# Kernel tuning notes

Hardware: AMD Instinct MI355X
Metric: run time of the kernel (lower is better)

## Reference

```python
import jax, jax.numpy as jnp
import numpy as np

N, E, F_IN, C = 50000, 800000, 128, 300
NEG_SLOPE = 0.2  # PyG GATv2Conv default negative_slope


def setup_inputs() -> dict:
    key = jax.random.key(0)
    ks = jax.random.split(key, 10)
    x = jax.random.normal(ks[0], (N, F_IN), dtype=jnp.float32)
    edge_index = jax.random.randint(ks[1], (2, E), 0, N, dtype=jnp.int64)
    s_in = np.float32(1.0 / np.sqrt(F_IN))
    s_c = np.float32(1.0 / np.sqrt(C))
    Wl = jax.random.normal(ks[2], (F_IN, C), dtype=jnp.float32) * s_in
    bl = jnp.zeros((C,), jnp.float32)
    Wr = jax.random.normal(ks[3], (F_IN, C), dtype=jnp.float32) * s_in
    br = jnp.zeros((C,), jnp.float32)
    att = jax.random.normal(ks[4], (C,), dtype=jnp.float32) * s_c
    bias = jnp.zeros((C,), jnp.float32)
    lw = jax.random.normal(ks[5], (C, 1), dtype=jnp.float32) * s_c
    lb = jnp.zeros((1,), jnp.float32)
    return {"x": x, "edge_index": edge_index, "Wl": Wl, "bl": bl,
            "Wr": Wr, "br": br, "att": att, "bias": bias, "lw": lw, "lb": lb}


def reference(x, edge_index, Wl, bl, Wr, br, att, bias, lw, lb):
    n = x.shape[0]
    # GATv2: separate source/target linear transforms
    xl = x @ Wl + bl  # [N, C] (source / message features)
    xr = x @ Wr + br  # [N, C] (target features)
    # add self loops (PyG default add_self_loops=True)
    loops = jnp.arange(n, dtype=edge_index.dtype)
    src = jnp.concatenate([edge_index[0], loops])  # [E+N]
    dst = jnp.concatenate([edge_index[1], loops])  # [E+N]
    # GATv2 attention logit: a^T LeakyReLU(xl_j + xr_i)
    e = jax.nn.leaky_relu(xl[src] + xr[dst], NEG_SLOPE) @ att  # [E+N]
    # segment softmax over incoming edges of each target node
    m = jax.ops.segment_max(e, dst, num_segments=n)
    ex = jnp.exp(e - m[dst])
    denom = jax.ops.segment_sum(ex, dst, num_segments=n)
    alpha = ex / denom[dst]  # [E+N]
    # weighted scatter-aggregation of source messages + conv bias
    out = jax.ops.segment_sum(xl[src] * alpha[:, None], dst, num_segments=n) + bias
    h = jax.nn.relu(out)          # torch.relu
    # F.dropout in eval mode is identity (reference is inference math)
    return jax.nn.sigmoid(h @ lw + lb)  # [N, 1]
```

## Files before the change

kernel.cpp:

```cpp
#include <hip/hip_runtime.h>
#include <hip/hip_fp16.h>

#define F_IN 128
#define C_DIM 300
#define NEG_SLOPE 0.2f
#define NCT  38
#define CH   8
#define NPB  256

typedef _Float16 half8 __attribute__((ext_vector_type(8)));
typedef _Float16 half4 __attribute__((ext_vector_type(4)));
typedef _Float16 h2    __attribute__((ext_vector_type(2)));
typedef float    f32x4 __attribute__((ext_vector_type(4)));
typedef float    f32x2 __attribute__((ext_vector_type(2)));

__device__ inline h2 as_h2(unsigned u) { union { unsigned u; h2 h; } c; c.u = u; return c.h; }
__device__ inline unsigned as_u(h2 h)  { union { unsigned u; h2 h; } c; c.h = h; return c.u; }
__device__ inline f32x2 upv(unsigned u) {
    h2 h = as_h2(u);
    f32x2 r; r.x = (float)h.x; r.y = (float)h.y; return r;
}

#if __has_builtin(__builtin_amdgcn_fdot2)
__device__ inline float fdot2w(h2 a, h2 b, float c) {
    return __builtin_amdgcn_fdot2(a, b, c, false);
}
#else
__device__ inline float fdot2w(h2 a, h2 b, float c) {
    return fmaf((float)a.y, (float)b.y, fmaf((float)a.x, (float)b.x, c));
}
#endif

__global__ __launch_bounds__(256) void convert_w(
    const float* __restrict__ Wl, const float* __restrict__ Wr,
    _Float16* __restrict__ Bp)
{
    int idx = blockIdx.x * 256 + threadIdx.x;
    if (idx >= 608 * F_IN) return;
    int nn = idx % 608;
    int k  = idx / 608;
    float v = 0.f;
    if (nn < 300)                   v = Wl[k * C_DIM + nn];
    else if (nn >= 304 && nn < 604) v = Wr[k * C_DIM + (nn - 304)];
    int ct = nn >> 4, n16 = nn & 15;
    int kr = k & 31,  ks  = k >> 5;
    int lane = ((kr >> 3) << 4) | n16;
    int j = k & 7;
    Bp[((((ct * 4 + ks) * 64) + lane) << 3) | j] = (_Float16)v;
}

__global__ __launch_bounds__(256) void gemm_xlxr(
    const float* __restrict__ x, const _Float16* __restrict__ Bp,
    const float* __restrict__ bl, const float* __restrict__ br,
    _Float16* __restrict__ xlh, _Float16* __restrict__ xrh, int n)
{
    __shared__ __align__(16) _Float16 xs[64][136];
    const int rb0 = blockIdx.x * 64;
    const int t   = threadIdx.x;

    #pragma unroll
    for (int i = 0; i < 8; ++i) {
        int flat = (i * 256 + t) * 4;
        int r = flat >> 7;
        int k = flat & 127;
        int gr = rb0 + r;
        if (gr >= n) gr = n - 1;
        float4 v = *reinterpret_cast<const float4*>(x + (size_t)gr * F_IN + k);
        half4 h = { (_Float16)v.x, (_Float16)v.y, (_Float16)v.z, (_Float16)v.w };
        *reinterpret_cast<half4*>(&xs[r][k]) = h;
    }
    __syncthreads();

    const int w    = t >> 6;
    const int lane = t & 63;
    const int m    = lane & 15;
    const int quad = lane >> 4;

    half8 a[4];
    #pragma unroll
    for (int ks = 0; ks < 4; ++ks)
        a[ks] = *reinterpret_cast<const half8*>(&xs[w * 16 + m][ks * 32 + quad * 8]);

    const int rbase = rb0 + w * 16 + quad * 4;

    #pragma unroll 2
    for (int ct = 0; ct < NCT; ++ct) {
        f32x4 acc = {0.f, 0.f, 0.f, 0.f};
        #pragma unroll
        for (int ks = 0; ks < 4; ++ks) {
            half8 b = *reinterpret_cast<const half8*>(
                Bp + (((size_t)(ct * 4 + ks) * 64 + lane) << 3));
            acc = __builtin_amdgcn_mfma_f32_16x16x32_f16(a[ks], b, acc, 0, 0, 0);
        }
        int col = ct * 16 + m;
        int isL = (col < 300);
        int isR = (col >= 304 && col < 604);
        if (isL | isR) {
            float bv = isL ? bl[col] : br[col - 304];
            _Float16* tab = isL ? (xlh + col) : (xrh + (col - 304));
            #pragma unroll
            for (int reg = 0; reg < 4; ++reg) {
                int row = rbase + reg;
                if (row < n)
                    tab[(size_t)row * C_DIM] = (_Float16)(acc[reg] + bv);
            }
        }
    }
}

__global__ __launch_bounds__(256) void bucket_count(
    const int* __restrict__ dst, unsigned* __restrict__ bcnt, int nE, int chunk4)
{
    __shared__ unsigned cnt[256];
    const int b = blockIdx.x, t = threadIdx.x;
    cnt[t] = 0;
    __syncthreads();
    const int4* dst4 = reinterpret_cast<const int4*>(dst);
    const int total4 = (nE + 3) >> 2;
    const int lo = b * chunk4;
    const int hi = min(total4, lo + chunk4);
    for (int i = lo + t; i < hi; i += 256) {
        int4 d = dst4[i];
        int e = i * 4;
        if (e + 3 < nE) {
            atomicAdd(&cnt[d.x >> 8], 1u);
            atomicAdd(&cnt[d.y >> 8], 1u);
            atomicAdd(&cnt[d.z >> 8], 1u);
            atomicAdd(&cnt[d.w >> 8], 1u);
        } else {
            if (e < nE)     atomicAdd(&cnt[d.x >> 8], 1u);
            if (e + 1 < nE) atomicAdd(&cnt[d.y >> 8], 1u);
            if (e + 2 < nE) atomicAdd(&cnt[d.z >> 8], 1u);
        }
    }
    __syncthreads();
    bcnt[t * NPB + b] = cnt[t];
}

__global__ __launch_bounds__(256) void scan_part(
    const unsigned* __restrict__ counts, unsigned* __restrict__ bsum, int n)
{
    __shared__ unsigned s[256];
    const int t = threadIdx.x;
    const int base = blockIdx.x * 1024 + t * 4;
    unsigned v = 0;
    #pragma unroll
    for (int i = 0; i < 4; ++i) {
        int idx = base + i;
        if (idx < n) v += counts[idx];
    }
    s[t] = v;
    __syncthreads();
    for (int off = 128; off > 0; off >>= 1) {
        if (t < off) s[t] += s[t + off];
        __syncthreads();
    }
    if (t == 0) bsum[blockIdx.x] = s[0];
}

__global__ __launch_bounds__(256) void scan_final(
    const unsigned* __restrict__ counts, const unsigned* __restrict__ bsum,
    unsigned* __restrict__ offs, int n, int nblk)
{
    __shared__ unsigned s[256];
    __shared__ unsigned sbase;
    const int t = threadIdx.x;
    if (t < 64) {
        unsigned v64 = (t < nblk) ? bsum[t] : 0u;
        unsigned inc = v64;
        #pragma unroll
        for (int off = 1; off < 64; off <<= 1) {
            unsigned u = __shfl_up(inc, off);
            if (t >= off) inc += u;
        }
        if (t == (int)blockIdx.x) sbase = inc - v64;
        if (blockIdx.x == gridDim.x - 1 && t == 63) offs[n] = inc;
    }
    const int base = blockIdx.x * 1024 + t * 4;
    unsigned c[4];
    unsigned v = 0;
    #pragma unroll
    for (int i = 0; i < 4; ++i) {
        int idx = base + i;
        c[i] = (idx < n) ? counts[idx] : 0u;
        v += c[i];
    }
    s[t] = v;
    __syncthreads();
    for (int off = 1; off < 256; off <<= 1) {
        unsigned u = (t >= off) ? s[t - off] : 0u;
        __syncthreads();
        if (t >= off) s[t] += u;
        __syncthreads();
    }
    unsigned run = sbase + s[t] - v;
    #pragma unroll
    for (int i = 0; i < 4; ++i) {
        int idx = base + i;
        if (idx < n) {
            offs[idx] = run;
            run += c[i];
        }
    }
}

__global__ __launch_bounds__(256) void partition_edges(
    const int* __restrict__ src, const int* __restrict__ dst,
    const unsigned* __restrict__ boff,
    unsigned* __restrict__ ebuf, int nE, int chunk4)
{
    __shared__ unsigned cur[256];
    const int b = blockIdx.x, t = threadIdx.x;
    cur[t] = boff[t * NPB + b];
    __syncthreads();
    const int4* dst4 = reinterpret_cast<const int4*>(dst);
    const int4* src4 = reinterpret_cast<const int4*>(src);
    const int total4 = (nE + 3) >> 2;
    const int lo = b * chunk4;
    const int hi = min(total4, lo + chunk4);
    for (int i = lo + t; i < hi; i += 256) {
        int4 d = dst4[i];
        int4 s = src4[i];
        int e = i * 4;
        int dv[4] = {d.x, d.y, d.z, d.w};
        int sv[4] = {s.x, s.y, s.z, s.w};
        #pragma unroll
        for (int j = 0; j < 4; ++j) {
            if (e + j < nE) {
                unsigned p = atomicAdd(&cur[dv[j] >> 8], 1u);
                ebuf[p] = (unsigned)sv[j] | ((unsigned)(dv[j] & 255) << 16);
            }
        }
    }
}

__global__ __launch_bounds__(256) void bucket_csr(
    const unsigned* __restrict__ ebuf, const unsigned* __restrict__ boff,
    unsigned* __restrict__ offs, int* __restrict__ csr_src, int n, int nE, int nb)
{
    __shared__ unsigned cnt[256];
    __shared__ unsigned s[256];
    __shared__ unsigned cur[256];
    const int bk = blockIdx.x;
    const int t  = threadIdx.x;
    const unsigned bstart = boff[(unsigned)bk * NPB];
    const unsigned bend   = boff[(unsigned)(bk + 1) * NPB];
    cnt[t] = 0;
    __syncthreads();
    for (unsigned i = bstart + t; i < bend; i += 256)
        atomicAdd(&cnt[(ebuf[i] >> 16) & 255], 1u);
    __syncthreads();
    unsigned v = cnt[t];
    s[t] = v;
    __syncthreads();
    for (int off = 1; off < 256; off <<= 1) {
        unsigned u = (t >= off) ? s[t - off] : 0u;
        __syncthreads();
        if (t >= off) s[t] += u;
        __syncthreads();
    }
    const unsigned excl = s[t] - v;
    const int node = (bk << 8) + t;
    if (node <= n) offs[node] = bstart + excl;
    if (t == 0 && bk == nb - 1 && (n & 255) == 0) offs[n] = (unsigned)nE;
    cur[t] = bstart + excl;
    __syncthreads();
    for (unsigned i = bstart + t; i < bend; i += 256) {
        unsigned e = ebuf[i];
        unsigned p = atomicAdd(&cur[(e >> 16) & 255], 1u);
        csr_src[p] = (int)(e & 0xFFFFu);
    }
}

__global__ __launch_bounds__(256) void gat_gather(
    const int* __restrict__ csr_src, const unsigned* __restrict__ offs,
    const _Float16* __restrict__ xlh, const _Float16* __restrict__ xrh,
    const float* __restrict__ att, const float* __restrict__ bias,
    const float* __restrict__ lw, const float* __restrict__ lb,
    float* __restrict__ y, int wlo, int whi)
{
    __shared__ __align__(16) float lds[4 * 560];
    float* part = lds + (threadIdx.x >> 6) * 560;

    const int wid  = wlo + ((blockIdx.x * blockDim.x + threadIdx.x) >> 6);
    const int lane = threadIdx.x & 63;
    if (wid >= whi) return;

    const int l2   = 2 * lane;
    const bool has2 = (lane < 22);
    const int t8   = lane & 7;
    const int o    = lane >> 3;
    const int byteoff = lane * 4;

    const _Float16* xrrow = xrh + (size_t)wid * C_DIM;
    h2 xr0 = *(const h2*)(xrrow + l2);
    h2 xr1 = *(const h2*)(xrrow + 128 + l2);
    h2 xr2 = {(_Float16)0, (_Float16)0};
    if (has2) xr2 = *(const h2*)(xrrow + 256 + l2);

    h2 a06[3], a04[3];
    #pragma unroll
    for (int k = 0; k < 3; ++k) {
        int c = 128 * k + l2;
        float ax = (c < C_DIM) ? att[c] : 0.f;
        float ay = (c + 1 < C_DIM) ? att[c + 1] : 0.f;
        a06[k].x = (_Float16)(0.6f * ax); a06[k].y = (_Float16)(0.6f * ay);
        a04[k].x = (_Float16)(0.4f * ax); a04[k].y = (_Float16)(0.4f * ay);
    }

    f32x2 acc2[3] = {{0.f, 0.f}, {0.f, 0.f}, {0.f, 0.f}};
    float den_l = 0.f;

    const unsigned start = offs[wid];
    const int totalE = (int)(offs[wid + 1] - start) + 1;
    const char* basep = (const char*)xlh;

    int idv = wid;
    {
        int k = lane;
        if (lane < CH && k > 0 && k < totalE) idv = csr_src[start + k - 1];
    }

    for (int base = 0; base < totalE; base += CH) {
        int rowb = idv * (C_DIM * 2);
        int ro[CH];
        #pragma unroll
        for (int tt = 0; tt < CH; ++tt) ro[tt] = __shfl(rowb, tt);

        unsigned pk0[CH], pk1[CH], pk2[CH];
        #pragma unroll
        for (int tt = 0; tt < CH; ++tt) {
            const char* p = basep + ro[tt] + byteoff;
            pk0[tt] = *(const unsigned*)(p);
            pk1[tt] = *(const unsigned*)(p + 256);
            pk2[tt] = 0u;
        }
        if (has2) {
            #pragma unroll
            for (int tt = 0; tt < CH; ++tt)
                pk2[tt] = *(const unsigned*)(basep + ro[tt] + byteoff + 512);
        }

        idv = wid;
        {
            int k = base + CH + lane;
            if (lane < CH && k > 0 && k < totalE) idv = csr_src[start + k - 1];
        }

        #pragma unroll
        for (int tt = 0; tt < CH; ++tt) {
            h2 z0 = as_h2(pk0[tt]) + xr0;
            h2 z1 = as_h2(pk1[tt]) + xr1;
            h2 z2 = as_h2(pk2[tt]) + xr2;
            float p = fdot2w(z0, a06[0], 0.f);
            p = fdot2w(as_h2(as_u(z0) & 0x7FFF7FFFu), a04[0], p);
            p = fdot2w(z1, a06[1], p);
            p = fdot2w(as_h2(as_u(z1) & 0x7FFF7FFFu), a04[1], p);
            p = fdot2w(z2, a06[2], p);
            p = fdot2w(as_h2(as_u(z2) & 0x7FFF7FFFu), a04[2], p);
            part[tt * 68 + lane] = p;
        }

        float wgt;
        {
            const int oo = (o + t8) & 7;
            const float* rp = part + t8 * 68 + oo * 8;
            float4 s0 = *(const float4*)(rp + 0);
            float4 s1 = *(const float4*)(rp + 4);
            float e = ((s0.x + s0.y) + (s0.z + s0.w)) + ((s1.x + s1.y) + (s1.z + s1.w));
            e += __shfl_xor(e, 8);
            e += __shfl_xor(e, 16);
            e += __shfl_xor(e, 32);
            bool valid = (base + t8) < totalE;
            wgt = valid ? __expf(fminf(e, 60.f)) : 0.f;
        }

        den_l += wgt;

        _Float16 wh = (_Float16)wgt;
        h2 wpair = {wh, wh};
        unsigned wbits = as_u(wpair);
        h2 hacc0 = {(_Float16)0, (_Float16)0};
        h2 hacc1 = {(_Float16)0, (_Float16)0};
        h2 hacc2 = {(_Float16)0, (_Float16)0};
        #pragma unroll
        for (int tt = 0; tt < CH; ++tt) {
            h2 wt2 = as_h2(__shfl(wbits, tt));
            hacc0 += wt2 * as_h2(pk0[tt]);
            hacc1 += wt2 * as_h2(pk1[tt]);
            hacc2 += wt2 * as_h2(pk2[tt]);
        }
        acc2[0] += upv(as_u(hacc0));
        acc2[1] += upv(as_u(hacc1));
        acc2[2] += upv(as_u(hacc2));
    }

    float den = den_l;
    den += __shfl_xor(den, 1);
    den += __shfl_xor(den, 2);
    den += __shfl_xor(den, 4);

    const float invd = 1.f / den;
    float dot = 0.f;
    #pragma unroll
    for (int k = 0; k < 3; ++k) {
        #pragma unroll
        for (int j = 0; j < 2; ++j) {
            int c = 128 * k + l2 + j;
            float b = (c < C_DIM) ? bias[c] : 0.f;
            float l = (c < C_DIM) ? lw[c] : 0.f;
            float a = (j == 0) ? acc2[k].x : acc2[k].y;
            float h = fmaf(a, invd, b);
            h = h > 0.f ? h : 0.f;
            dot = fmaf(h, l, dot);
        }
    }
    #pragma unroll
    for (int off = 32; off; off >>= 1) dot += __shfl_xor(dot, off);
    if (lane == 0) y[wid] = 1.f / (1.f + __expf(-(dot + lb[0])));
}

extern "C" void kernel_launch(void* const* d_in, const int* in_sizes, int n_in,
                              void* d_out, int out_size, void* d_ws, size_t ws_size,
                              hipStream_t stream)
{
    const float* x    = (const float*)d_in[0];
    const int*   ei   = (const int*)d_in[1];
    const float* Wl   = (const float*)d_in[2];
    const float* bl   = (const float*)d_in[3];
    const float* Wr   = (const float*)d_in[4];
    const float* br   = (const float*)d_in[5];
    const float* att  = (const float*)d_in[6];
    const float* bias = (const float*)d_in[7];
    const float* lw   = (const float*)d_in[8];
    const float* lb   = (const float*)d_in[9];
    float* y = (float*)d_out;

    const int n  = in_sizes[0] / F_IN;
    const int nE = in_sizes[1] / 2;
    const int* src_arr = ei;
    const int* dst_arr = ei + nE;

    const int NB     = (n + 255) >> 8;
    const int total4 = (nE + 3) >> 2;
    const int chunk4 = (total4 + NPB - 1) / NPB;
    const int M      = 256 * NPB;
    const int nblkM  = (M + 1023) / 1024;

    _Float16* xlh      = (_Float16*)d_ws;
    _Float16* xrh      = xlh + (size_t)n * C_DIM;
    _Float16* Bp       = xrh + (size_t)n * C_DIM;
    unsigned* bcnt     = (unsigned*)(Bp + NCT * 4 * 64 * 8);
    unsigned* boff     = bcnt + M;
    unsigned* offs     = boff + (M + 1);
    unsigned* bsum     = offs + (n + 1);
    int*      csr_src  = (int*)(bsum + 64);
    unsigned* ebuf     = (unsigned*)(csr_src + nE);

    convert_w<<<(608 * F_IN + 255) / 256, 256, 0, stream>>>(Wl, Wr, Bp);

    bucket_count<<<NPB, 256, 0, stream>>>(dst_arr, bcnt, nE, chunk4);
    scan_part<<<nblkM, 256, 0, stream>>>(bcnt, bsum, M);
    scan_final<<<nblkM, 256, 0, stream>>>(bcnt, bsum, boff, M, nblkM);
    partition_edges<<<NPB, 256, 0, stream>>>(src_arr, dst_arr, boff, ebuf, nE, chunk4);
    bucket_csr<<<NB, 256, 0, stream>>>(ebuf, boff, offs, csr_src, n, nE, NB);

    gemm_xlxr<<<(n + 63) / 64, 256, 0, stream>>>(x, Bp, bl, br, xlh, xrh, n);

    const int p1 = n / 3, p2 = 2 * (n / 3);
    gat_gather<<<((p1 - 0) + 3) / 4, 256, 0, stream>>>(csr_src, offs, xlh, xrh, att, bias, lw, lb, y, 0, p1);
    gat_gather<<<((p2 - p1) + 3) / 4, 256, 0, stream>>>(csr_src, offs, xlh, xrh, att, bias, lw, lb, y, p1, p2);
    gat_gather<<<((n - p2) + 3) / 4, 256, 0, stream>>>(csr_src, offs, xlh, xrh, att, bias, lw, lb, y, p2, n);
}
```

Baseline: 258.4 us.

## Split GEMM column tiles across two blocks, prefetch B, merge gather launches

The xl/xr GEMM now launches twice as many blocks, and each block handles half of the 38 column tiles (19 each). This raises parallelism, at the cost of converting and staging each block's x rows to LDS twice. Inside the column loop, the B fragments for the next tile are loaded ahead of the MFMAs for the current one, to hide global load latency. The three gat_gather launches over node thirds are folded into one launch covering all nodes, which removes launch overhead and tail gaps between them.

```diff
diff --git a/kernel.cpp b/kernel.cpp
--- a/kernel.cpp
+++ b/kernel.cpp
@@ -5,6 +5,7 @@
 #define C_DIM 300
 #define NEG_SLOPE 0.2f
 #define NCT  38
+#define CTH  19
 #define CH   8
 #define NPB  256
 
@@ -55,7 +56,9 @@
     _Float16* __restrict__ xlh, _Float16* __restrict__ xrh, int n)
 {
     __shared__ __align__(16) _Float16 xs[64][136];
-    const int rb0 = blockIdx.x * 64;
+    const int rg  = blockIdx.x >> 1;
+    const int cs  = blockIdx.x & 1;
+    const int rb0 = rg * 64;
     const int t   = threadIdx.x;
 
     #pragma unroll
@@ -82,16 +85,28 @@
         a[ks] = *reinterpret_cast<const half8*>(&xs[w * 16 + m][ks * 32 + quad * 8]);
 
     const int rbase = rb0 + w * 16 + quad * 4;
-
-    #pragma unroll 2
-    for (int ct = 0; ct < NCT; ++ct) {
+    const int ct0   = cs * CTH;
+
+    const half8* bp = reinterpret_cast<const half8*>(Bp) ;
+    half8 bc0 = bp[((size_t)(ct0 * 4 + 0) * 64) + lane];
+    half8 bc1 = bp[((size_t)(ct0 * 4 + 1) * 64) + lane];
+    half8 bc2 = bp[((size_t)(ct0 * 4 + 2) * 64) + lane];
+    half8 bc3 = bp[((size_t)(ct0 * 4 + 3) * 64) + lane];
+
+    for (int ci = 0; ci < CTH; ++ci) {
+        const int ct  = ct0 + ci;
+        const int ctn = (ci < CTH - 1) ? ct + 1 : ct;
+        half8 bn0 = bp[((size_t)(ctn * 4 + 0) * 64) + lane];
+        half8 bn1 = bp[((size_t)(ctn * 4 + 1) * 64) + lane];
+        half8 bn2 = bp[((size_t)(ctn * 4 + 2) * 64) + lane];
+        half8 bn3 = bp[((size_t)(ctn * 4 + 3) * 64) + lane];
+
         f32x4 acc = {0.f, 0.f, 0.f, 0.f};
-        #pragma unroll
-        for (int ks = 0; ks < 4; ++ks) {
-            half8 b = *reinterpret_cast<const half8*>(
-                Bp + (((size_t)(ct * 4 + ks) * 64 + lane) << 3));
-            acc = __builtin_amdgcn_mfma_f32_16x16x32_f16(a[ks], b, acc, 0, 0, 0);
-        }
+        acc = __builtin_amdgcn_mfma_f32_16x16x32_f16(a[0], bc0, acc, 0, 0, 0);
+        acc = __builtin_amdgcn_mfma_f32_16x16x32_f16(a[1], bc1, acc, 0, 0, 0);
+        acc = __builtin_amdgcn_mfma_f32_16x16x32_f16(a[2], bc2, acc, 0, 0, 0);
+        acc = __builtin_amdgcn_mfma_f32_16x16x32_f16(a[3], bc3, acc, 0, 0, 0);
+
         int col = ct * 16 + m;
         int isL = (col < 300);
         int isR = (col >= 304 && col < 604);
@@ -105,6 +120,7 @@
                     tab[(size_t)row * C_DIM] = (_Float16)(acc[reg] + bv);
             }
         }
+        bc0 = bn0; bc1 = bn1; bc2 = bn2; bc3 = bn3;
     }
 }
 
@@ -277,14 +293,14 @@
     const _Float16* __restrict__ xlh, const _Float16* __restrict__ xrh,
     const float* __restrict__ att, const float* __restrict__ bias,
     const float* __restrict__ lw, const float* __restrict__ lb,
-    float* __restrict__ y, int wlo, int whi)
+    float* __restrict__ y, int n)
 {
     __shared__ __align__(16) float lds[4 * 560];
     float* part = lds + (threadIdx.x >> 6) * 560;
 
-    const int wid  = wlo + ((blockIdx.x * blockDim.x + threadIdx.x) >> 6);
+    const int wid  = (blockIdx.x * blockDim.x + threadIdx.x) >> 6;
     const int lane = threadIdx.x & 63;
-    if (wid >= whi) return;
+    if (wid >= n) return;
 
     const int l2   = 2 * lane;
     const bool has2 = (lane < 22);
@@ -465,10 +481,7 @@
     partition_edges<<<NPB, 256, 0, stream>>>(src_arr, dst_arr, boff, ebuf, nE, chunk4);
     bucket_csr<<<NB, 256, 0, stream>>>(ebuf, boff, offs, csr_src, n, nE, NB);
 
-    gemm_xlxr<<<(n + 63) / 64, 256, 0, stream>>>(x, Bp, bl, br, xlh, xrh, n);
-
-    const int p1 = n / 3, p2 = 2 * (n / 3);
-    gat_gather<<<((p1 - 0) + 3) / 4, 256, 0, stream>>>(csr_src, offs, xlh, xrh, att, bias, lw, lb, y, 0, p1);
-    gat_gather<<<((p2 - p1) + 3) / 4, 256, 0, stream>>>(csr_src, offs, xlh, xrh, att, bias, lw, lb, y, p1, p2);
-    gat_gather<<<((n - p2) + 3) / 4, 256, 0, stream>>>(csr_src, offs, xlh, xrh, att, bias, lw, lb, y, p2, n);
-}
+    gemm_xlxr<<<((n + 63) / 64) * 2, 256, 0, stream>>>(x, Bp, bl, br, xlh, xrh, n);
+
+    gat_gather<<<(n + 3) / 4, 256, 0, stream>>>(csr_src, offs, xlh, xrh, att, bias, lw, lb, y, n);
+}
```

New measurement: 229.9 us. 11.0% less time.
